# Kernel tuning notes

Measured on AMD Instinct MI355X. Metric: run time of the kernel, lower is better.

## Reference

```python
import jax, jax.numpy as jnp
import numpy as np

B, H, W = 32, 56, 56
C_IN, C_OUT, GROUPS, K = 256, 256, 32, 3
EPS = 1e-5


def setup_inputs() -> dict:
    key = jax.random.key(0)
    k1, k2 = jax.random.split(key, 2)
    x = jax.random.normal(k1, (B, H, W, C_IN), dtype=jnp.float32)
    # HWIO grouped-conv kernel: I = C_IN // GROUPS = 8; equivalent to the
    # concatenation of the 32 per-group [3,3,8,8] Conv2d kernels along O.
    w = jax.random.normal(k2, (K, K, C_IN // GROUPS, C_OUT), dtype=jnp.float32) * 0.05
    b = jnp.zeros((C_OUT,), dtype=jnp.float32)
    gamma = jnp.ones((C_OUT,), dtype=jnp.float32)
    beta = jnp.zeros((C_OUT,), dtype=jnp.float32)
    return {"x": x, "w": w, "b": b, "gamma": gamma, "beta": beta}


def reference(x, w, b, gamma, beta):
    # Grouped conv: same math as tf.split -> per-group Conv2d -> tf.concat,
    # expressed as one native grouped convolution (feature_group_count).
    y = jax.lax.conv_general_dilated(
        x, w,
        window_strides=(1, 1),
        padding="SAME",
        dimension_numbers=("NHWC", "HWIO", "NHWC"),
        feature_group_count=GROUPS,
    ) + b  # [B,H,W,C_OUT]
    # BatchNorm (training forward: batch statistics over N,H,W per channel)
    mean = jnp.mean(y, axis=(0, 1, 2))
    var = jnp.var(y, axis=(0, 1, 2))
    y = (y - mean) * jax.lax.rsqrt(var + EPS) * gamma + beta
    # Act('relu')
    return jax.nn.relu(y)
```

## Files before the change

### kernel.cpp

```cpp
#include <hip/hip_runtime.h>
#include <hip/hip_bf16.h>

#define BB 32
#define HH 56
#define WW 56
#define CC 256
#define NPIX (BB*HH*WW)
#define EPS 1e-5f

typedef short bf16x8 __attribute__((ext_vector_type(8)));
typedef float f32x4  __attribute__((ext_vector_type(4)));

__device__ __forceinline__ unsigned short f2bf(float f) {
    __hip_bfloat16 h = __float2bfloat16(f);
    return *reinterpret_cast<unsigned short*>(&h);
}


__global__ void k0_zero(float* stats) { stats[threadIdx.x] = 0.f; }

__global__ __launch_bounds__(256) void k1_conv(
    const float* __restrict__ x, const float* __restrict__ wgt,
    __hip_bfloat16* __restrict__ y, float* __restrict__ stats)
{
    __shared__ unsigned short xt[10*58*24];
    __shared__ unsigned short wb[16*160];
    __shared__ float bsum[16], bsq[16];

    const int gp = blockIdx.x;
    const int hb = blockIdx.y;
    const int b  = blockIdx.z;
    const int t  = threadIdx.x;
    const int h0 = hb * 8;

    if (t < 16) { bsum[t] = 0.f; bsq[t] = 0.f; }

    float4 v[10];
    int    off[10];
    #pragma unroll
    for (int j = 0; j < 10; ++j) {
        const int i   = j*256 + t;
        const int ci4 = i & 3;
        const int cq  = i >> 2;
        const int row = cq / 58;
        const int col = cq - row*58;
        const int hh  = h0 - 1 + row;
        const int wc  = col - 1;
        off[j] = (row*58 + col)*24 + ci4*4;
        v[j] = make_float4(0.f, 0.f, 0.f, 0.f);
        if (i < 2320 && (unsigned)hh < HH && (unsigned)wc < WW)
            v[j] = *(const float4*)(x + (((size_t)(b*HH + hh)*WW + wc)*CC + gp*16 + ci4*4));
    }
    {
        const int n  = t >> 4;
        const int k0 = t & 15;
        #pragma unroll
        for (int j = 0; j < 10; ++j) {
            const int kk  = k0 + j*16;
            const int g   = (kk >= 80);
            const int r   = kk - g*80;
            const int tap = r >> 3, ci = r & 7;
            unsigned short val = 0;
            if (tap < 9 && (n >> 3) == g)
                val = f2bf(wgt[(tap*8 + ci)*CC + gp*16 + n]);
            wb[n*160 + kk] = val;
        }
    }
    #pragma unroll
    for (int j = 0; j < 10; ++j) {
        if (j*256 + t < 2320) {
            ushort4 s;
            s.x = f2bf(v[j].x); s.y = f2bf(v[j].y);
            s.z = f2bf(v[j].z); s.w = f2bf(v[j].w);
            *(ushort4*)(xt + off[j]) = s;
        }
    }
    __syncthreads();

    const int lane = t & 63;
    const int rp   = t >> 6;
    const int n    = lane & 15;
    const int q    = lane >> 4;
    const int m    = lane & 15;
    const int rowr = rp*2 + (m >> 3);
    const int colb = m & 7;

    bf16x8 bfrag[5];
    #pragma unroll
    for (int s = 0; s < 5; ++s)
        bfrag[s] = *(const bf16x8*)(wb + n*160 + s*32 + q*8);

    int aoff[5];
    #pragma unroll
    for (int s = 0; s < 5; ++s) {
        int o  = s*4 + q;
        int g  = (o >= 10);
        int tp = o - g*10;
        if (tp == 9) tp = 0;
        int dh = tp / 3, dw = tp - dh*3;
        aoff[s] = ((rowr + dh)*58 + colb + dw)*24 + g*8;
    }

    const int hq = q >> 1;
    const int wq = (q & 1) * 4;
    float lsum = 0.f, lsq = 0.f;

    #pragma unroll 2
    for (int ct = 0; ct < 7; ++ct) {
        f32x4 acc = {0.f, 0.f, 0.f, 0.f};
        #pragma unroll
        for (int s = 0; s < 5; ++s) {
            bf16x8 af = *(const bf16x8*)(xt + aoff[s] + ct*192);
            acc = __builtin_amdgcn_mfma_f32_16x16x32_bf16(af, bfrag[s], acc, 0, 0, 0);
        }
        const int h = h0 + rp*2 + hq;
        const size_t base = (((size_t)(b*HH + h))*WW + ct*8 + wq)*CC + gp*16 + n;
        #pragma unroll
        for (int i = 0; i < 4; ++i) {
            float vv = acc[i];
            y[base + (size_t)i*CC] = __float2bfloat16(vv);
            lsum += vv;
            lsq  += vv * vv;
        }
    }

    atomicAdd(&bsum[n], lsum);
    atomicAdd(&bsq[n],  lsq);
    __syncthreads();
    if (t < 16) {
        atomicAdd(&stats[gp*16 + t],       bsum[t]);
        atomicAdd(&stats[256 + gp*16 + t], bsq[t]);
    }
}

__global__ void k2_finalize(const float* __restrict__ stats,
                            const float* __restrict__ gamma,
                            const float* __restrict__ beta,
                            float* __restrict__ ss)
{
    int c = threadIdx.x;
    float inv_n = 1.f / (float)NPIX;
    float mean = stats[c] * inv_n;
    float var  = stats[256 + c] * inv_n - mean * mean;
    float scale = gamma[c] * rsqrtf(var + EPS);
    ss[c]       = scale;
    ss[256 + c] = beta[c] - mean * scale;
}

__global__ __launch_bounds__(256) void k3_norm(
    const __hip_bfloat16* __restrict__ y, const float* __restrict__ ss,
    float* __restrict__ out)
{
    const int t   = threadIdx.x;
    const int oct = t & 31;
    const int pr  = t >> 5;
    const int c0  = oct * 8;

    float4 sc0 = *(const float4*)(ss + c0);
    float4 sc1 = *(const float4*)(ss + c0 + 4);
    float4 sh0 = *(const float4*)(ss + 256 + c0);
    float4 sh1 = *(const float4*)(ss + 256 + c0 + 4);

    const uint4* yv = (const uint4*)y;
    float4* ov = (float4*)out;
    const int px0 = blockIdx.x * 32 + pr;

    uint4 d[4];
    #pragma unroll
    for (int i = 0; i < 4; ++i)
        d[i] = yv[(size_t)(px0 + i*8)*32 + oct];

    #pragma unroll
    for (int i = 0; i < 4; ++i) {
        const int px = px0 + i*8;
        float f0 = __uint_as_float((d[i].x & 0xffffu) << 16);
        float f1 = __uint_as_float(d[i].x & 0xffff0000u);
        float f2 = __uint_as_float((d[i].y & 0xffffu) << 16);
        float f3 = __uint_as_float(d[i].y & 0xffff0000u);
        float f4 = __uint_as_float((d[i].z & 0xffffu) << 16);
        float f5 = __uint_as_float(d[i].z & 0xffff0000u);
        float f6 = __uint_as_float((d[i].w & 0xffffu) << 16);
        float f7 = __uint_as_float(d[i].w & 0xffff0000u);

        float4 o0, o1;
        o0.x = fmaxf(0.f, f0 * sc0.x + sh0.x);
        o0.y = fmaxf(0.f, f1 * sc0.y + sh0.y);
        o0.z = fmaxf(0.f, f2 * sc0.z + sh0.z);
        o0.w = fmaxf(0.f, f3 * sc0.w + sh0.w);
        o1.x = fmaxf(0.f, f4 * sc1.x + sh1.x);
        o1.y = fmaxf(0.f, f5 * sc1.y + sh1.y);
        o1.z = fmaxf(0.f, f6 * sc1.z + sh1.z);
        o1.w = fmaxf(0.f, f7 * sc1.w + sh1.w);

        ov[(size_t)px*64 + oct*2]     = o0;
        ov[(size_t)px*64 + oct*2 + 1] = o1;
    }
}

extern "C" void kernel_launch(void* const* d_in, const int* in_sizes, int n_in,
                              void* d_out, int out_size, void* d_ws, size_t ws_size,
                              hipStream_t stream) {
    const float* x     = (const float*)d_in[0];
    const float* wgt   = (const float*)d_in[1];
    const float* gamma = (const float*)d_in[3];
    const float* beta  = (const float*)d_in[4];
    float* out = (float*)d_out;

    float* stats = (float*)d_ws;
    float* ss    = (float*)((char*)d_ws + 2048);
    __hip_bfloat16* y = (__hip_bfloat16*)((char*)d_ws + 4096);

    k0_zero<<<1, 512, 0, stream>>>(stats);
    k1_conv<<<dim3(16, 7, BB), 256, 0, stream>>>(x, wgt, y, stats);
    k2_finalize<<<1, 256, 0, stream>>>(stats, gamma, beta, ss);
    k3_norm<<<NPIX/32, 256, 0, stream>>>(y, ss, out);
}
```

Baseline: 250.0 us.

## Double-buffer conv input tiles, fold finalize into norm, use memset and nontemporal stores

```diff
diff --git a/kernel.cpp b/kernel.cpp
--- a/kernel.cpp
+++ b/kernel.cpp
@@ -10,6 +10,9 @@
 
 typedef short bf16x8 __attribute__((ext_vector_type(8)));
 typedef float f32x4  __attribute__((ext_vector_type(4)));
+typedef unsigned int u32;
+
+#define ROWB 1872
 
 __device__ __forceinline__ unsigned short f2bf(float f) {
     __hip_bfloat16 h = __float2bfloat16(f);
@@ -17,26 +20,42 @@
 }
 
 
-__global__ void k0_zero(float* stats) { stats[threadIdx.x] = 0.f; }
-
-__global__ __launch_bounds__(256) void k1_conv(
+__global__ __launch_bounds__(256, 3) void k1_conv(
     const float* __restrict__ x, const float* __restrict__ wgt,
     __hip_bfloat16* __restrict__ y, float* __restrict__ stats)
 {
-    __shared__ unsigned short xt[10*58*24];
+    __shared__ __align__(16) unsigned char xbuf[2][10*ROWB];
     __shared__ unsigned short wb[16*160];
     __shared__ float bsum[16], bsq[16];
 
-    const int gp = blockIdx.x;
-    const int hb = blockIdx.y;
-    const int b  = blockIdx.z;
-    const int t  = threadIdx.x;
-    const int h0 = hb * 8;
+    const int gp   = blockIdx.x;
+    const int b    = blockIdx.y;
+    const int hz   = blockIdx.z;
+    const int t    = threadIdx.x;
+    const int lane = t & 63;
+    const int wv   = t >> 6;
+    const int k0h  = hz*4, nb = 4 - hz;
 
     if (t < 16) { bsum[t] = 0.f; bsq[t] = 0.f; }
 
-    float4 v[10];
-    int    off[10];
+    {
+        const int n  = t >> 4;
+        const int kq = t & 15;
+        #pragma unroll
+        for (int j = 0; j < 10; ++j) {
+            const int kk = kq + j*16;
+            const int g  = (kk >= 80);
+            const int r  = kk - g*80;
+            const int tap = r >> 3, ci = r & 7;
+            unsigned short val = 0;
+            if (tap < 9 && (n >> 3) == g)
+                val = f2bf(wgt[(tap*8 + ci)*CC + gp*16 + n]);
+            wb[n*160 + kk] = val;
+        }
+    }
+
+    int goff[10], soff[10];
+    int mfull = 0, mfirst = 0, mlast = 0;
     #pragma unroll
     for (int j = 0; j < 10; ++j) {
         const int i   = j*256 + t;
@@ -44,53 +63,23 @@
         const int cq  = i >> 2;
         const int row = cq / 58;
         const int col = cq - row*58;
-        const int hh  = h0 - 1 + row;
-        const int wc  = col - 1;
-        off[j] = (row*58 + col)*24 + ci4*4;
-        v[j] = make_float4(0.f, 0.f, 0.f, 0.f);
-        if (i < 2320 && (unsigned)hh < HH && (unsigned)wc < WW)
-            v[j] = *(const float4*)(x + (((size_t)(b*HH + hh)*WW + wc)*CC + gp*16 + ci4*4));
-    }
-    {
-        const int n  = t >> 4;
-        const int k0 = t & 15;
-        #pragma unroll
-        for (int j = 0; j < 10; ++j) {
-            const int kk  = k0 + j*16;
-            const int g   = (kk >= 80);
-            const int r   = kk - g*80;
-            const int tap = r >> 3, ci = r & 7;
-            unsigned short val = 0;
-            if (tap < 9 && (n >> 3) == g)
-                val = f2bf(wgt[(tap*8 + ci)*CC + gp*16 + n]);
-            wb[n*160 + kk] = val;
-        }
-    }
-    #pragma unroll
-    for (int j = 0; j < 10; ++j) {
-        if (j*256 + t < 2320) {
-            ushort4 s;
-            s.x = f2bf(v[j].x); s.y = f2bf(v[j].y);
-            s.z = f2bf(v[j].z); s.w = f2bf(v[j].w);
-            *(ushort4*)(xt + off[j]) = s;
-        }
-    }
-    __syncthreads();
-
-    const int lane = t & 63;
-    const int rp   = t >> 6;
+        goff[j] = ((row - 1)*WW + (col - 1))*CC + ci4*4;
+        soff[j] = row*ROWB + col*32 + ci4*8;
+        const bool ok = (i < 2320) && (col >= 1) && (col <= 56);
+        if (ok) {
+            mfull |= 1 << j;
+            if (row != 0) mfirst |= 1 << j;
+            if (row != 9) mlast  |= 1 << j;
+        }
+    }
+    const int xbase = b*HH*WW*CC + gp*16;
+
     const int n    = lane & 15;
     const int q    = lane >> 4;
     const int m    = lane & 15;
-    const int rowr = rp*2 + (m >> 3);
+    const int rowr = wv*2 + (m >> 3);
     const int colb = m & 7;
-
-    bf16x8 bfrag[5];
-    #pragma unroll
-    for (int s = 0; s < 5; ++s)
-        bfrag[s] = *(const bf16x8*)(wb + n*160 + s*32 + q*8);
-
-    int aoff[5];
+    int aoffB[5];
     #pragma unroll
     for (int s = 0; s < 5; ++s) {
         int o  = s*4 + q;
@@ -98,30 +87,94 @@
         int tp = o - g*10;
         if (tp == 9) tp = 0;
         int dh = tp / 3, dw = tp - dh*3;
-        aoff[s] = ((rowr + dh)*58 + colb + dw)*24 + g*8;
-    }
-
+        aoffB[s] = (rowr + dh)*ROWB + (colb + dw)*32 + g*16;
+    }
     const int hq = q >> 1;
     const int wq = (q & 1) * 4;
+
+    float4 v[10];
+    {
+        const float* gx = x + xbase + k0h*8*WW*CC;
+        const int msk = (k0h == 0) ? mfirst : mfull;
+        #pragma unroll
+        for (int j = 0; j < 10; ++j) {
+            v[j] = make_float4(0.f, 0.f, 0.f, 0.f);
+            if ((msk >> j) & 1) v[j] = *(const float4*)(gx + goff[j]);
+        }
+    }
+    #pragma unroll
+    for (int j = 0; j < 10; ++j) {
+        if (j*256 + t < 2320) {
+            u32 a0 = __float_as_uint(v[j].x) + 0x8000u;
+            u32 a1 = __float_as_uint(v[j].y) + 0x8000u;
+            u32 a2 = __float_as_uint(v[j].z) + 0x8000u;
+            u32 a3 = __float_as_uint(v[j].w) + 0x8000u;
+            uint2 pk;
+            pk.x = __builtin_amdgcn_perm(a1, a0, 0x07060302u);
+            pk.y = __builtin_amdgcn_perm(a3, a2, 0x07060302u);
+            *(uint2*)(&xbuf[0][0] + soff[j]) = pk;
+        }
+    }
+    __syncthreads();
+
+    bf16x8 bfrag[5];
+    #pragma unroll
+    for (int s = 0; s < 5; ++s)
+        bfrag[s] = *(const bf16x8*)(wb + n*160 + s*32 + q*8);
+
     float lsum = 0.f, lsq = 0.f;
 
-    #pragma unroll 2
-    for (int ct = 0; ct < 7; ++ct) {
-        f32x4 acc = {0.f, 0.f, 0.f, 0.f};
+    for (int kk = 0; kk < nb; ++kk) {
+        const int k = k0h + kk;
+        const unsigned char* cur = &xbuf[kk & 1][0];
+        unsigned char* nxt = &xbuf[(kk & 1) ^ 1][0];
+        const bool more = (kk + 1 < nb);
+
+        if (more) {
+            const float* gx = x + xbase + (k + 1)*8*WW*CC;
+            const int msk = (k + 1 == 6) ? mlast : mfull;
+            #pragma unroll
+            for (int j = 0; j < 10; ++j) {
+                v[j] = make_float4(0.f, 0.f, 0.f, 0.f);
+                if ((msk >> j) & 1) v[j] = *(const float4*)(gx + goff[j]);
+            }
+        }
+
         #pragma unroll
-        for (int s = 0; s < 5; ++s) {
-            bf16x8 af = *(const bf16x8*)(xt + aoff[s] + ct*192);
-            acc = __builtin_amdgcn_mfma_f32_16x16x32_bf16(af, bfrag[s], acc, 0, 0, 0);
-        }
-        const int h = h0 + rp*2 + hq;
-        const size_t base = (((size_t)(b*HH + h))*WW + ct*8 + wq)*CC + gp*16 + n;
-        #pragma unroll
-        for (int i = 0; i < 4; ++i) {
-            float vv = acc[i];
-            y[base + (size_t)i*CC] = __float2bfloat16(vv);
-            lsum += vv;
-            lsq  += vv * vv;
-        }
+        for (int ct = 0; ct < 7; ++ct) {
+            f32x4 acc = {0.f, 0.f, 0.f, 0.f};
+            #pragma unroll
+            for (int s = 0; s < 5; ++s) {
+                bf16x8 af = *(const bf16x8*)(cur + aoffB[s] + ct*256);
+                acc = __builtin_amdgcn_mfma_f32_16x16x32_bf16(af, bfrag[s], acc, 0, 0, 0);
+            }
+            const int h = k*8 + wv*2 + hq;
+            const size_t base = (((size_t)(b*HH + h))*WW + ct*8 + wq)*CC + gp*16 + n;
+            #pragma unroll
+            for (int i = 0; i < 4; ++i) {
+                float vv = acc[i];
+                y[base + (size_t)i*CC] = __float2bfloat16(vv);
+                lsum += vv;
+                lsq  += vv * vv;
+            }
+        }
+
+        if (more) {
+            #pragma unroll
+            for (int j = 0; j < 10; ++j) {
+                if (j*256 + t < 2320) {
+                    u32 a0 = __float_as_uint(v[j].x) + 0x8000u;
+                    u32 a1 = __float_as_uint(v[j].y) + 0x8000u;
+                    u32 a2 = __float_as_uint(v[j].z) + 0x8000u;
+                    u32 a3 = __float_as_uint(v[j].w) + 0x8000u;
+                    uint2 pk;
+                    pk.x = __builtin_amdgcn_perm(a1, a0, 0x07060302u);
+                    pk.y = __builtin_amdgcn_perm(a3, a2, 0x07060302u);
+                    *(uint2*)(nxt + soff[j]) = pk;
+                }
+            }
+        }
+        __syncthreads();
     }
 
     atomicAdd(&bsum[n], lsum);
@@ -133,45 +186,42 @@
     }
 }
 
-__global__ void k2_finalize(const float* __restrict__ stats,
-                            const float* __restrict__ gamma,
-                            const float* __restrict__ beta,
-                            float* __restrict__ ss)
-{
-    int c = threadIdx.x;
-    float inv_n = 1.f / (float)NPIX;
-    float mean = stats[c] * inv_n;
-    float var  = stats[256 + c] * inv_n - mean * mean;
-    float scale = gamma[c] * rsqrtf(var + EPS);
-    ss[c]       = scale;
-    ss[256 + c] = beta[c] - mean * scale;
-}
-
 __global__ __launch_bounds__(256) void k3_norm(
-    const __hip_bfloat16* __restrict__ y, const float* __restrict__ ss,
+    const __hip_bfloat16* __restrict__ y, const float* __restrict__ stats,
+    const float* __restrict__ gamma, const float* __restrict__ beta,
     float* __restrict__ out)
 {
-    const int t   = threadIdx.x;
+    __shared__ float lss[512];
+    const int t = threadIdx.x;
+    {
+        const float inv_n = 1.f / (float)NPIX;
+        float mean = stats[t] * inv_n;
+        float var  = stats[256 + t] * inv_n - mean * mean;
+        float sc   = gamma[t] * rsqrtf(var + EPS);
+        lss[t]       = sc;
+        lss[256 + t] = beta[t] - mean * sc;
+    }
+    __syncthreads();
+
     const int oct = t & 31;
     const int pr  = t >> 5;
     const int c0  = oct * 8;
 
-    float4 sc0 = *(const float4*)(ss + c0);
-    float4 sc1 = *(const float4*)(ss + c0 + 4);
-    float4 sh0 = *(const float4*)(ss + 256 + c0);
-    float4 sh1 = *(const float4*)(ss + 256 + c0 + 4);
+    float4 sc0 = *(const float4*)(lss + c0);
+    float4 sc1 = *(const float4*)(lss + c0 + 4);
+    float4 sh0 = *(const float4*)(lss + 256 + c0);
+    float4 sh1 = *(const float4*)(lss + 256 + c0 + 4);
 
     const uint4* yv = (const uint4*)y;
-    float4* ov = (float4*)out;
-    const int px0 = blockIdx.x * 32 + pr;
-
-    uint4 d[4];
-    #pragma unroll
-    for (int i = 0; i < 4; ++i)
+    const int px0 = blockIdx.x * 16 + pr;
+
+    uint4 d[2];
+    #pragma unroll
+    for (int i = 0; i < 2; ++i)
         d[i] = yv[(size_t)(px0 + i*8)*32 + oct];
 
     #pragma unroll
-    for (int i = 0; i < 4; ++i) {
+    for (int i = 0; i < 2; ++i) {
         const int px = px0 + i*8;
         float f0 = __uint_as_float((d[i].x & 0xffffu) << 16);
         float f1 = __uint_as_float(d[i].x & 0xffff0000u);
@@ -182,18 +232,19 @@
         float f6 = __uint_as_float((d[i].w & 0xffffu) << 16);
         float f7 = __uint_as_float(d[i].w & 0xffff0000u);
 
-        float4 o0, o1;
-        o0.x = fmaxf(0.f, f0 * sc0.x + sh0.x);
-        o0.y = fmaxf(0.f, f1 * sc0.y + sh0.y);
-        o0.z = fmaxf(0.f, f2 * sc0.z + sh0.z);
-        o0.w = fmaxf(0.f, f3 * sc0.w + sh0.w);
-        o1.x = fmaxf(0.f, f4 * sc1.x + sh1.x);
-        o1.y = fmaxf(0.f, f5 * sc1.y + sh1.y);
-        o1.z = fmaxf(0.f, f6 * sc1.z + sh1.z);
-        o1.w = fmaxf(0.f, f7 * sc1.w + sh1.w);
-
-        ov[(size_t)px*64 + oct*2]     = o0;
-        ov[(size_t)px*64 + oct*2 + 1] = o1;
+        f32x4 o0, o1;
+        o0[0] = fmaxf(0.f, f0 * sc0.x + sh0.x);
+        o0[1] = fmaxf(0.f, f1 * sc0.y + sh0.y);
+        o0[2] = fmaxf(0.f, f2 * sc0.z + sh0.z);
+        o0[3] = fmaxf(0.f, f3 * sc0.w + sh0.w);
+        o1[0] = fmaxf(0.f, f4 * sc1.x + sh1.x);
+        o1[1] = fmaxf(0.f, f5 * sc1.y + sh1.y);
+        o1[2] = fmaxf(0.f, f6 * sc1.z + sh1.z);
+        o1[3] = fmaxf(0.f, f7 * sc1.w + sh1.w);
+
+        f32x4* op = (f32x4*)out + (size_t)px*64 + oct*2;
+        __builtin_nontemporal_store(o0, op);
+        __builtin_nontemporal_store(o1, op + 1);
     }
 }
 
@@ -207,11 +258,9 @@
     float* out = (float*)d_out;
 
     float* stats = (float*)d_ws;
-    float* ss    = (float*)((char*)d_ws + 2048);
     __hip_bfloat16* y = (__hip_bfloat16*)((char*)d_ws + 4096);
 
-    k0_zero<<<1, 512, 0, stream>>>(stats);
-    k1_conv<<<dim3(16, 7, BB), 256, 0, stream>>>(x, wgt, y, stats);
-    k2_finalize<<<1, 256, 0, stream>>>(stats, gamma, beta, ss);
-    k3_norm<<<NPIX/32, 256, 0, stream>>>(y, ss, out);
-}
+    hipMemsetAsync(stats, 0, 2048, stream);
+    k1_conv<<<dim3(16, BB, 2), 256, 0, stream>>>(x, wgt, y, stats);
+    k3_norm<<<NPIX/16, 256, 0, stream>>>(y, stats, gamma, beta, out);
+}
```

Result: slower. 255.4 us (+2.2%).
